# Kernel tuning notes

Measured on AMD Instinct MI355X. Metric: run time of the kernel, lower is better.

The kernel has to match this reference:

```python
import jax, jax.numpy as jnp
import numpy as np

SEQ_LEN = 4096
D_IN = 2048
D_OUT = 2048
DROPOUT_P = 0.5


def setup_inputs() -> dict:
    key = jax.random.key(0)
    kx, kq, kk, kv = jax.random.split(key, 4)
    return {
        "x": jax.random.normal(kx, (SEQ_LEN, D_IN), dtype=jnp.float32),
        "W_query": jax.random.uniform(kq, (D_IN, D_OUT), dtype=jnp.float32),
        "W_key": jax.random.uniform(kk, (D_IN, D_OUT), dtype=jnp.float32),
        "W_value": jax.random.uniform(kv, (D_IN, D_OUT), dtype=jnp.float32),
    }


def reference(x, W_query, W_key, W_value):
    # projections: [S, d_in] @ [d_in, d_out] -> [S, d_out]
    queries = x @ W_query
    keys = x @ W_key
    values = x @ W_value
    # full score matrix [S, S]
    attn_scores = queries @ keys.T
    S = attn_scores.shape[0]
    causal_mask = jnp.triu(jnp.ones((S, S), dtype=bool), k=1)
    masked = jnp.where(causal_mask, -jnp.inf, attn_scores)
    scale = jnp.sqrt(jnp.asarray(keys.shape[-1], dtype=masked.dtype))
    attn_weights = jax.nn.softmax(masked / scale, axis=1)
    # dropout p=0.5 (train mode), inverted scaling, deterministic key
    keep = jax.random.bernoulli(jax.random.key(42), 1.0 - DROPOUT_P, attn_weights.shape)
    attn_weights = jnp.where(keep, attn_weights / (1.0 - DROPOUT_P), 0.0)
    context_vec = attn_weights @ values  # [S, d_out]
    return context_vec
```

## Files before the change

### kernel.cpp

```cpp
#include <hip/hip_runtime.h>
#include <cstdint>
#include <cstddef>
#include <cmath>

#define SEQ 4096
#define DM  2048

typedef unsigned int u32;
typedef unsigned short u16;
typedef __attribute__((ext_vector_type(8))) short bf16x8;
typedef __attribute__((ext_vector_type(4))) float f32x4;

__device__ __forceinline__ u16 f2bf(float f) {
  u32 u = __float_as_uint(f);
  return (u16)((u + 0x7FFFu + ((u >> 16) & 1u)) >> 16);
}
__device__ __forceinline__ float bf2f(u16 h) { return __uint_as_float(((u32)h) << 16); }

__device__ __forceinline__ u32 rotl32(u32 x, int r) { return (x << r) | (x >> (32 - r)); }

__device__ __forceinline__ void tf2x32(u32 c0, u32 c1, u32& o0, u32& o1) {
  const u32 k0 = 0u, k1 = 42u, k2 = 0x1BD11BDAu ^ 0u ^ 42u;
  u32 x0 = c0 + k0;
  u32 x1 = c1 + k1;
#define TFR(r) { x0 += x1; x1 = rotl32(x1, (r)); x1 ^= x0; }
  TFR(13) TFR(15) TFR(26) TFR(6)   x0 += k1; x1 += k2 + 1u;
  TFR(17) TFR(29) TFR(16) TFR(24)  x0 += k2; x1 += k0 + 2u;
  TFR(13) TFR(15) TFR(26) TFR(6)   x0 += k0; x1 += k1 + 3u;
  TFR(17) TFR(29) TFR(16) TFR(24)  x0 += k1; x1 += k2 + 4u;
  TFR(13) TFR(15) TFR(26) TFR(6)   x0 += k2; x1 += k0 + 5u;
#undef TFR
  o0 = x0; o1 = x1;
}

__device__ __forceinline__ bool dropout_keep(u32 idx) {
  u32 a, b; tf2x32(0u, idx, a, b);
  return (((a ^ b) & 0x80000000u) == 0u);
}

__device__ __forceinline__ void g2l16(const void* g, void* l) {
  __builtin_amdgcn_global_load_lds((const __attribute__((address_space(1))) u32*)g,
                                   (__attribute__((address_space(3))) u32*)l, 16, 0, 0);
}

#define MFMA16(a, b, c) __builtin_amdgcn_mfma_f32_16x16x32_bf16(a, b, c, 0, 0, 0)


__device__ __forceinline__ void gemm_core_split(
    const u16* __restrict__ Ah, const u16* __restrict__ AlFT,
    const u16* __restrict__ Bh, const u16* __restrict__ BlFT,
    int lda, int ldb, int rowBlock, int colBlock, int kmax,
    f32x4 (&acc)[4][4], u16* smem)
{
  u16* Als = smem;
  u16* Bls = smem + 4096;
  const int tid  = threadIdx.x;
  const int wid  = tid >> 6;
  const int lane = tid & 63;
  const int wr   = (wid & 1) << 6;
  const int wc   = (wid >> 1) << 6;
  const int lrow = lane & 15;
  const int lk   = (((lane >> 4) ^ ((lrow >> 1) & 3)) << 3);
  const int srow = wid * 32 + (lane >> 2);
  const int skol = (((lane & 3) ^ ((lane >> 3) & 3)) << 3);
  const int KA32 = lda >> 5, KB32 = ldb >> 5;
  const int rtA = (rowBlock >> 4) + ((wid & 1) << 2);
  const int rtB = (colBlock >> 4) + ((wid >> 1) << 2);

  const f32x4 zero = {0.f, 0.f, 0.f, 0.f};
#pragma unroll
  for (int i = 0; i < 4; ++i)
#pragma unroll
    for (int j = 0; j < 4; ++j) acc[i][j] = zero;

  for (int kb = 0; kb < kmax; kb += 32) {
    const int kt = kb >> 5;
    bf16x8 al[4], bl[4];
#pragma unroll
    for (int r = 0; r < 4; ++r) {
      al[r] = *(const bf16x8*)(AlFT + (((size_t)(rtA + r) * KA32 + kt) * 64 + lane) * 8);
      bl[r] = *(const bf16x8*)(BlFT + (((size_t)(rtB + r) * KB32 + kt) * 64 + lane) * 8);
    }
#pragma unroll
    for (int t = 0; t < 2; ++t) {
      const size_t ga = (size_t)(rowBlock + srow + t * 16) * lda + kb + skol;
      const size_t gb = (size_t)(colBlock + srow + t * 16) * ldb + kb + skol;
      const int lo = (wid * 32 + t * 16) * 32;
      g2l16(Ah + ga, &Als[lo]);
      g2l16(Bh + gb, &Bls[lo]);
    }
    __syncthreads();

    bf16x8 ah[4], bh[4];
#pragma unroll
    for (int r = 0; r < 4; ++r) {
      ah[r] = *(const bf16x8*)&Als[(wr + r * 16 + lrow) * 32 + lk];
      bh[r] = *(const bf16x8*)&Bls[(wc + r * 16 + lrow) * 32 + lk];
    }
#pragma unroll
    for (int r = 0; r < 4; ++r)
#pragma unroll
      for (int c = 0; c < 4; ++c) {
        acc[r][c] = MFMA16(ah[r], bh[c], acc[r][c]);
        acc[r][c] = MFMA16(ah[r], bl[c], acc[r][c]);
        acc[r][c] = MFMA16(al[r], bh[c], acc[r][c]);
      }
    __syncthreads();
  }
}

__device__ __forceinline__ void gemm_core(
    const u16* __restrict__ Ah, const u16* __restrict__ Bh,
    int lda, int ldb, int rowBlock, int colBlock, int kmax,
    f32x4 (&acc)[4][4])
{
  __shared__ __align__(16) u16 Als[128 * 32];
  __shared__ __align__(16) u16 Bls[128 * 32];
  const int tid  = threadIdx.x;
  const int wid  = tid >> 6;
  const int lane = tid & 63;
  const int wr   = (wid & 1) << 6;
  const int wc   = (wid >> 1) << 6;
  const int lrow = lane & 15;
  const int lk   = (((lane >> 4) ^ ((lrow >> 1) & 3)) << 3);
  const int srow = wid * 32 + (lane >> 2);
  const int skol = (((lane & 3) ^ ((lane >> 3) & 3)) << 3);

  const f32x4 zero = {0.f, 0.f, 0.f, 0.f};
#pragma unroll
  for (int i = 0; i < 4; ++i)
#pragma unroll
    for (int j = 0; j < 4; ++j) acc[i][j] = zero;

  for (int kb = 0; kb < kmax; kb += 32) {
#pragma unroll
    for (int t = 0; t < 2; ++t) {
      const size_t ga = (size_t)(rowBlock + srow + t * 16) * lda + kb + skol;
      const size_t gb = (size_t)(colBlock + srow + t * 16) * ldb + kb + skol;
      const int lo = (wid * 32 + t * 16) * 32;
      g2l16(Ah + ga, &Als[lo]);
      g2l16(Bh + gb, &Bls[lo]);
    }
    __syncthreads();

    bf16x8 ah[4], bh[4];
#pragma unroll
    for (int r = 0; r < 4; ++r) {
      ah[r] = *(const bf16x8*)&Als[(wr + r * 16 + lrow) * 32 + lk];
      bh[r] = *(const bf16x8*)&Bls[(wc + r * 16 + lrow) * 32 + lk];
    }
#pragma unroll
    for (int r = 0; r < 4; ++r)
#pragma unroll
      for (int c = 0; c < 4; ++c)
        acc[r][c] = MFMA16(ah[r], bh[c], acc[r][c]);
    __syncthreads();
  }
}

__global__ __launch_bounds__(256) void k_split_x(const float* __restrict__ X,
                                                 u16* __restrict__ Xh, u16* __restrict__ Xl) {
  const int wid = threadIdx.x >> 6, lane = threadIdx.x & 63;
  const int kt = blockIdx.x;
  const int rt = blockIdx.y * 4 + wid;
  const int row = rt * 16 + (lane & 15);
  const int col = kt * 32 + ((lane >> 4) << 3);
  const float* src = X + (size_t)row * DM + col;
  const float4 v0 = *(const float4*)src;
  const float4 v1 = *(const float4*)(src + 4);
  float v[8] = {v0.x, v0.y, v0.z, v0.w, v1.x, v1.y, v1.z, v1.w};
  u16 h[8], l[8];
#pragma unroll
  for (int j = 0; j < 8; ++j) {
    h[j] = f2bf(v[j]);
    l[j] = f2bf(v[j] - bf2f(h[j]));
  }
  u16* hp = Xh + (size_t)row * DM + col;
  *(ushort4*)hp = *(ushort4*)&h[0];
  *(ushort4*)(hp + 4) = *(ushort4*)&h[4];
  u16* lp = Xl + (((size_t)rt * 64 + kt) * 64 + lane) * 8;
  *(ushort4*)lp = *(ushort4*)&l[0];
  *(ushort4*)(lp + 4) = *(ushort4*)&l[4];
}

__global__ __launch_bounds__(256) void k_split_w(
    const float* __restrict__ Wq, const float* __restrict__ Wk, const float* __restrict__ Wv,
    u16* __restrict__ Wqh, u16* __restrict__ Wql,
    u16* __restrict__ Wkh, u16* __restrict__ Wkl, u16* __restrict__ Wvh) {
  const int z = blockIdx.z;
  const float* W = (z == 0) ? Wq : (z == 1) ? Wk : Wv;
  u16* Oh = (z == 0) ? Wqh : (z == 1) ? Wkh : Wvh;
  u16* Ol = (z == 0) ? Wql : Wkl;
  __shared__ float t[64][65];
  const int tid = threadIdx.x;
  const int n0 = blockIdx.x * 64, k0 = blockIdx.y * 64;
  const int tx = tid & 63, ty = tid >> 6;
#pragma unroll
  for (int i = 0; i < 16; ++i)
    t[ty * 16 + i][tx] = W[(size_t)(k0 + ty * 16 + i) * DM + n0 + tx];
  __syncthreads();
  {
    const int nl = tid >> 2, kc = (tid & 3) * 16;
    u16 h[16];
#pragma unroll
    for (int i = 0; i < 16; ++i) h[i] = f2bf(t[kc + i][nl]);
    u16* hp = Oh + (size_t)(n0 + nl) * DM + k0 + kc;
#pragma unroll
    for (int i = 0; i < 4; ++i) *(ushort4*)(hp + i * 4) = *(ushort4*)&h[i * 4];
  }
  if (z < 2) {
    const int wid = tid >> 6, lane = tid & 63;
#pragma unroll
    for (int kt = 0; kt < 2; ++kt) {
      const int nl = wid * 16 + (lane & 15);
      const int kc = kt * 32 + ((lane >> 4) << 3);
      u16 l[8];
#pragma unroll
      for (int j = 0; j < 8; ++j) {
        const float v = t[kc + j][nl];
        l[j] = f2bf(v - bf2f(f2bf(v)));
      }
      const int rtg = (n0 >> 4) + wid, ktg = (k0 >> 5) + kt;
      u16* lp = Ol + (((size_t)rtg * 64 + ktg) * 64 + lane) * 8;
      *(ushort4*)lp = *(ushort4*)&l[0];
      *(ushort4*)(lp + 4) = *(ushort4*)&l[4];
    }
  }
}

__global__ __launch_bounds__(256) void k_proj_qk(
    const u16* __restrict__ Xh, const u16* __restrict__ Xl,
    const u16* __restrict__ Wqh, const u16* __restrict__ Wql,
    const u16* __restrict__ Wkh, const u16* __restrict__ Wkl,
    u16* __restrict__ Qh, u16* __restrict__ Ql,
    u16* __restrict__ Kh, u16* __restrict__ Kl, float rscaleQ)
{
  __shared__ __align__(16) u16 smem[128 * 128];
  const int z = blockIdx.z;
  const u16* Bh = z ? Wkh : Wqh;
  const u16* Bl = z ? Wkl : Wql;
  u16* Oh = z ? Kh : Qh;
  u16* Ol = z ? Kl : Ql;
  const float rs = z ? 1.0f : rscaleQ;
  const int rowBlock = blockIdx.y * 128, colBlock = blockIdx.x * 128;
  f32x4 acc[4][4];
  gemm_core_split(Xh, Xl, Bh, Bl, DM, DM, rowBlock, colBlock, DM, acc, smem);

  const int lane = threadIdx.x & 63, wid = threadIdx.x >> 6;
  const int lr0 = ((wid & 1) << 6) + ((lane >> 4) << 2);
  const int lc0 = ((wid >> 1) << 6) + (lane & 15);
#pragma unroll
  for (int r = 0; r < 4; ++r)
#pragma unroll
    for (int c = 0; c < 4; ++c)
#pragma unroll
      for (int e = 0; e < 4; ++e) {
        const float v = acc[r][c][e] * rs;
        const u16 h = f2bf(v);
        const int lrow = lr0 + r * 16 + e, lcol = lc0 + c * 16;
        Oh[(size_t)(rowBlock + lrow) * DM + colBlock + lcol] = h;
        smem[lrow * 128 + lcol] = f2bf(v - bf2f(h));
      }
  __syncthreads();
#pragma unroll
  for (int t8 = 0; t8 < 8; ++t8) {
    const int idx = wid * 8 + t8;
    const int rt = idx >> 2, kt = idx & 3;
    u16 l[8];
#pragma unroll
    for (int j = 0; j < 8; ++j)
      l[j] = smem[(rt * 16 + (lane & 15)) * 128 + kt * 32 + ((lane >> 4) << 3) + j];
    const int rtg = (rowBlock >> 4) + rt, ktg = (colBlock >> 5) + kt;
    u16* lp = Ol + (((size_t)rtg * (DM / 32) + ktg) * 64 + lane) * 8;
    *(ushort4*)lp = *(ushort4*)&l[0];
    *(ushort4*)(lp + 4) = *(ushort4*)&l[4];
  }
}

__global__ __launch_bounds__(256) void k_proj_v(
    const u16* __restrict__ Xh, const u16* __restrict__ Wvh, u16* __restrict__ Vt)
{
  f32x4 acc[4][4];
  gemm_core(Xh, Wvh, DM, DM, blockIdx.y * 128, blockIdx.x * 128, DM, acc);

  const int lane = threadIdx.x & 63, wid = threadIdx.x >> 6;
  const int r0 = blockIdx.y * 128 + ((wid & 1) << 6) + ((lane >> 4) << 2);
  const int c0 = blockIdx.x * 128 + ((wid >> 1) << 6) + (lane & 15);
#pragma unroll
  for (int r = 0; r < 4; ++r)
#pragma unroll
    for (int c = 0; c < 4; ++c) {
      const int d = c0 + c * 16;
      const int s0 = r0 + r * 16;
      ushort4 pk;
      pk.x = f2bf(acc[r][c][0]); pk.y = f2bf(acc[r][c][1]);
      pk.z = f2bf(acc[r][c][2]); pk.w = f2bf(acc[r][c][3]);
      *(ushort4*)(Vt + (size_t)d * SEQ + s0) = pk;
    }
}

__global__ __launch_bounds__(256) void k_scores(
    const u16* __restrict__ Qh, const u16* __restrict__ Ql,
    const u16* __restrict__ Kh, const u16* __restrict__ Kl, float* __restrict__ S)
{
  __shared__ __align__(16) u16 smem[128 * 64];
  const int bid = blockIdx.x;
  int by = (int)((sqrtf(8.0f * (float)bid + 1.0f) - 1.0f) * 0.5f);
  while ((by + 1) * (by + 2) / 2 <= bid) ++by;
  while (by * (by + 1) / 2 > bid) --by;
  const int bx = bid - by * (by + 1) / 2;

  f32x4 acc[4][4];
  gemm_core_split(Qh, Ql, Kh, Kl, DM, DM, by * 128, bx * 128, DM, acc, smem);

  const int lane = threadIdx.x & 63, wid = threadIdx.x >> 6;
  const int r0 = by * 128 + ((wid & 1) << 6) + ((lane >> 4) << 2);
  const int c0 = bx * 128 + ((wid >> 1) << 6) + (lane & 15);
#pragma unroll
  for (int r = 0; r < 4; ++r)
#pragma unroll
    for (int c = 0; c < 4; ++c)
#pragma unroll
      for (int e = 0; e < 4; ++e)
        S[(size_t)(r0 + r * 16 + e) * SEQ + (c0 + c * 16)] = acc[r][c][e];
}

__global__ __launch_bounds__(256) void k_softmax_dropout(const float* __restrict__ S,
                                                         u16* __restrict__ P) {
  const int row = blockIdx.x;
  const int n = row + 1;
  const int nt = (n + 1023) >> 10;
  const int tid = threadIdx.x;
  __shared__ float buf[SEQ];
  __shared__ float red[4];
  __shared__ float bcast;
  const float* srow = S + (size_t)row * SEQ;

  float lmax = -INFINITY;
  for (int t = 0; t < nt; ++t) {
    int j4 = tid + t * 256;
    float4 v = *(const float4*)(srow + (size_t)j4 * 4);
    int b = j4 * 4;
    float x0 = (b + 0 < n) ? v.x : -INFINITY;
    float x1 = (b + 1 < n) ? v.y : -INFINITY;
    float x2 = (b + 2 < n) ? v.z : -INFINITY;
    float x3 = (b + 3 < n) ? v.w : -INFINITY;
    buf[b + 0] = x0; buf[b + 1] = x1; buf[b + 2] = x2; buf[b + 3] = x3;
    lmax = fmaxf(lmax, fmaxf(fmaxf(x0, x1), fmaxf(x2, x3)));
  }
  for (int off = 32; off > 0; off >>= 1) lmax = fmaxf(lmax, __shfl_down(lmax, off, 64));
  if ((tid & 63) == 0) red[tid >> 6] = lmax;
  __syncthreads();
  if (tid == 0) bcast = fmaxf(fmaxf(red[0], red[1]), fmaxf(red[2], red[3]));
  __syncthreads();
  const float m = bcast;

  float lsum = 0.f;
  for (int t = 0; t < nt; ++t) {
    int b = (tid + t * 256) * 4;
    float e0 = expf(buf[b + 0] - m);
    float e1 = expf(buf[b + 1] - m);
    float e2 = expf(buf[b + 2] - m);
    float e3 = expf(buf[b + 3] - m);
    buf[b + 0] = e0; buf[b + 1] = e1; buf[b + 2] = e2; buf[b + 3] = e3;
    lsum += (e0 + e1) + (e2 + e3);
  }
  for (int off = 32; off > 0; off >>= 1) lsum += __shfl_down(lsum, off, 64);
  if ((tid & 63) == 0) red[tid >> 6] = lsum;
  __syncthreads();
  if (tid == 0) bcast = (red[0] + red[1]) + (red[2] + red[3]);
  __syncthreads();
  const float total = bcast;

  u16* prow = P + (size_t)row * SEQ;
  const int zeroEnd = ((row >> 7) + 1) << 7;
  for (int j = tid; j < zeroEnd; j += 256) {
    float out = 0.f;
    if (j < n) {
      const float w = buf[j] / total;
      out = dropout_keep((u32)(row * SEQ + j)) ? w * 2.0f : 0.f;
    }
    prow[j] = f2bf(out);
  }
}

__global__ __launch_bounds__(256) void k_pv(const u16* __restrict__ P,
                                            const u16* __restrict__ Vt,
                                            float* __restrict__ O) {
  const int by = (SEQ / 128 - 1) - blockIdx.y;
  f32x4 acc[4][4];
  gemm_core(P, Vt, SEQ, SEQ, by * 128, blockIdx.x * 128, (by + 1) * 128, acc);

  const int lane = threadIdx.x & 63, wid = threadIdx.x >> 6;
  const int r0 = by * 128 + ((wid & 1) << 6) + ((lane >> 4) << 2);
  const int c0 = blockIdx.x * 128 + ((wid >> 1) << 6) + (lane & 15);
#pragma unroll
  for (int r = 0; r < 4; ++r)
#pragma unroll
    for (int c = 0; c < 4; ++c)
#pragma unroll
      for (int e = 0; e < 4; ++e)
        O[(size_t)(r0 + r * 16 + e) * DM + (c0 + c * 16)] = acc[r][c][e];
}

extern "C" void kernel_launch(void* const* d_in, const int* in_sizes, int n_in,
                              void* d_out, int out_size, void* d_ws, size_t ws_size,
                              hipStream_t stream) {
  const float* x  = (const float*)d_in[0];
  const float* Wq = (const float*)d_in[1];
  const float* Wk = (const float*)d_in[2];
  const float* Wv = (const float*)d_in[3];

  const size_t PL = (size_t)SEQ * DM;
  const size_t WL = (size_t)DM * DM;
  u16* base = (u16*)d_ws;
  u16* Qh = base;
  u16* Ql = Qh + PL;
  u16* Kh = Ql + PL;
  u16* Kl = Kh + PL;
  u16* Vt = Kl + PL;
  u16* P  = base;
  u16* regA = Vt + PL;
  u16* Xh  = regA;
  u16* Xl  = Xh + PL;
  u16* Wqh = Xl + PL;
  u16* Wql = Wqh + WL;
  u16* Wkh = Wql + WL;
  u16* Wkl = Wkh + WL;
  u16* Wvh = Wkl + WL;
  float* S = (float*)regA;

  const float rscale = 1.0f / sqrtf(2048.0f);
  dim3 blk(256);
  k_split_x<<<dim3(DM / 32, SEQ / 64), blk, 0, stream>>>(x, Xh, Xl);
  k_split_w<<<dim3(DM / 64, DM / 64, 3), blk, 0, stream>>>(Wq, Wk, Wv, Wqh, Wql, Wkh, Wkl, Wvh);
  k_proj_qk<<<dim3(DM / 128, SEQ / 128, 2), blk, 0, stream>>>(Xh, Xl, Wqh, Wql, Wkh, Wkl,
                                                              Qh, Ql, Kh, Kl, rscale);
  k_proj_v<<<dim3(DM / 128, SEQ / 128), blk, 0, stream>>>(Xh, Wvh, Vt);
  k_scores<<<dim3((SEQ / 128) * (SEQ / 128 + 1) / 2), blk, 0, stream>>>(Qh, Ql, Kh, Kl, S);
  k_softmax_dropout<<<dim3(SEQ), blk, 0, stream>>>(S, P);
  k_pv<<<dim3(DM / 128, SEQ / 128), blk, 0, stream>>>(P, Vt, (float*)d_out);
}
```

Measured before the change: 681.5 us.

## Double K-step per barrier in GEMM cores and merge split/projection kernels

Both GEMM cores now stage two 32-wide K slices into LDS per iteration, a 64-wide K step, so they run half as many barrier pairs, at the cost of twice the shared memory. The split kernels for x and the weights are merged into one launch, and the V projection is folded into the Q/K projection kernel as a third z-slice. The aim is fewer launches and better occupancy and tail behaviour. The bigger LDS footprint may reduce how many blocks fit per CU.

```diff
diff --git a/kernel.cpp b/kernel.cpp
--- a/kernel.cpp
+++ b/kernel.cpp
@@ -5,6 +5,7 @@
 
 #define SEQ 4096
 #define DM  2048
+#define NSC ((SEQ / 128) * (SEQ / 128 + 1) / 2)
 
 typedef unsigned int u32;
 typedef unsigned short u16;
@@ -53,7 +54,7 @@
     f32x4 (&acc)[4][4], u16* smem)
 {
   u16* Als = smem;
-  u16* Bls = smem + 4096;
+  u16* Bls = smem + 8192;
   const int tid  = threadIdx.x;
   const int wid  = tid >> 6;
   const int lane = tid & 63;
@@ -73,38 +74,39 @@
 #pragma unroll
     for (int j = 0; j < 4; ++j) acc[i][j] = zero;
 
-  for (int kb = 0; kb < kmax; kb += 32) {
-    const int kt = kb >> 5;
-    bf16x8 al[4], bl[4];
-#pragma unroll
-    for (int r = 0; r < 4; ++r) {
-      al[r] = *(const bf16x8*)(AlFT + (((size_t)(rtA + r) * KA32 + kt) * 64 + lane) * 8);
-      bl[r] = *(const bf16x8*)(BlFT + (((size_t)(rtB + r) * KB32 + kt) * 64 + lane) * 8);
+  for (int kb = 0; kb < kmax; kb += 64) {
+#pragma unroll
+    for (int h = 0; h < 2; ++h)
+#pragma unroll
+      for (int t = 0; t < 2; ++t) {
+        const size_t ga = (size_t)(rowBlock + srow + t * 16) * lda + kb + h * 32 + skol;
+        const size_t gb = (size_t)(colBlock + srow + t * 16) * ldb + kb + h * 32 + skol;
+        const int lo = h * 4096 + (wid * 32 + t * 16) * 32;
+        g2l16(Ah + ga, &Als[lo]);
+        g2l16(Bh + gb, &Bls[lo]);
+      }
+    __syncthreads();
+
+#pragma unroll
+    for (int h = 0; h < 2; ++h) {
+      const int kt = (kb >> 5) + h;
+      bf16x8 al[4], bl[4], ah[4], bh[4];
+#pragma unroll
+      for (int r = 0; r < 4; ++r) {
+        al[r] = *(const bf16x8*)(AlFT + (((size_t)(rtA + r) * KA32 + kt) * 64 + lane) * 8);
+        bl[r] = *(const bf16x8*)(BlFT + (((size_t)(rtB + r) * KB32 + kt) * 64 + lane) * 8);
+        ah[r] = *(const bf16x8*)&Als[h * 4096 + (wr + r * 16 + lrow) * 32 + lk];
+        bh[r] = *(const bf16x8*)&Bls[h * 4096 + (wc + r * 16 + lrow) * 32 + lk];
+      }
+#pragma unroll
+      for (int r = 0; r < 4; ++r)
+#pragma unroll
+        for (int c = 0; c < 4; ++c) {
+          acc[r][c] = MFMA16(ah[r], bh[c], acc[r][c]);
+          acc[r][c] = MFMA16(ah[r], bl[c], acc[r][c]);
+          acc[r][c] = MFMA16(al[r], bh[c], acc[r][c]);
+        }
     }
-#pragma unroll
-    for (int t = 0; t < 2; ++t) {
-      const size_t ga = (size_t)(rowBlock + srow + t * 16) * lda + kb + skol;
-      const size_t gb = (size_t)(colBlock + srow + t * 16) * ldb + kb + skol;
-      const int lo = (wid * 32 + t * 16) * 32;
-      g2l16(Ah + ga, &Als[lo]);
-      g2l16(Bh + gb, &Bls[lo]);
-    }
-    __syncthreads();
-
-    bf16x8 ah[4], bh[4];
-#pragma unroll
-    for (int r = 0; r < 4; ++r) {
-      ah[r] = *(const bf16x8*)&Als[(wr + r * 16 + lrow) * 32 + lk];
-      bh[r] = *(const bf16x8*)&Bls[(wc + r * 16 + lrow) * 32 + lk];
-    }
-#pragma unroll
-    for (int r = 0; r < 4; ++r)
-#pragma unroll
-      for (int c = 0; c < 4; ++c) {
-        acc[r][c] = MFMA16(ah[r], bh[c], acc[r][c]);
-        acc[r][c] = MFMA16(ah[r], bl[c], acc[r][c]);
-        acc[r][c] = MFMA16(al[r], bh[c], acc[r][c]);
-      }
     __syncthreads();
   }
 }
@@ -112,10 +114,10 @@
 __device__ __forceinline__ void gemm_core(
     const u16* __restrict__ Ah, const u16* __restrict__ Bh,
     int lda, int ldb, int rowBlock, int colBlock, int kmax,
-    f32x4 (&acc)[4][4])
+    f32x4 (&acc)[4][4], u16* smem)
 {
-  __shared__ __align__(16) u16 Als[128 * 32];
-  __shared__ __align__(16) u16 Bls[128 * 32];
+  u16* Als = smem;
+  u16* Bls = smem + 8192;
   const int tid  = threadIdx.x;
   const int wid  = tid >> 6;
   const int lane = tid & 63;
@@ -132,68 +134,78 @@
 #pragma unroll
     for (int j = 0; j < 4; ++j) acc[i][j] = zero;
 
-  for (int kb = 0; kb < kmax; kb += 32) {
-#pragma unroll
-    for (int t = 0; t < 2; ++t) {
-      const size_t ga = (size_t)(rowBlock + srow + t * 16) * lda + kb + skol;
-      const size_t gb = (size_t)(colBlock + srow + t * 16) * ldb + kb + skol;
-      const int lo = (wid * 32 + t * 16) * 32;
-      g2l16(Ah + ga, &Als[lo]);
-      g2l16(Bh + gb, &Bls[lo]);
+  for (int kb = 0; kb < kmax; kb += 64) {
+#pragma unroll
+    for (int h = 0; h < 2; ++h)
+#pragma unroll
+      for (int t = 0; t < 2; ++t) {
+        const size_t ga = (size_t)(rowBlock + srow + t * 16) * lda + kb + h * 32 + skol;
+        const size_t gb = (size_t)(colBlock + srow + t * 16) * ldb + kb + h * 32 + skol;
+        const int lo = h * 4096 + (wid * 32 + t * 16) * 32;
+        g2l16(Ah + ga, &Als[lo]);
+        g2l16(Bh + gb, &Bls[lo]);
+      }
+    __syncthreads();
+
+#pragma unroll
+    for (int h = 0; h < 2; ++h) {
+      bf16x8 ah[4], bh[4];
+#pragma unroll
+      for (int r = 0; r < 4; ++r) {
+        ah[r] = *(const bf16x8*)&Als[h * 4096 + (wr + r * 16 + lrow) * 32 + lk];
+        bh[r] = *(const bf16x8*)&Bls[h * 4096 + (wc + r * 16 + lrow) * 32 + lk];
+      }
+#pragma unroll
+      for (int r = 0; r < 4; ++r)
+#pragma unroll
+        for (int c = 0; c < 4; ++c)
+          acc[r][c] = MFMA16(ah[r], bh[c], acc[r][c]);
     }
     __syncthreads();
-
-    bf16x8 ah[4], bh[4];
-#pragma unroll
-    for (int r = 0; r < 4; ++r) {
-      ah[r] = *(const bf16x8*)&Als[(wr + r * 16 + lrow) * 32 + lk];
-      bh[r] = *(const bf16x8*)&Bls[(wc + r * 16 + lrow) * 32 + lk];
-    }
-#pragma unroll
-    for (int r = 0; r < 4; ++r)
-#pragma unroll
-      for (int c = 0; c < 4; ++c)
-        acc[r][c] = MFMA16(ah[r], bh[c], acc[r][c]);
-    __syncthreads();
-  }
-}
-
-__global__ __launch_bounds__(256) void k_split_x(const float* __restrict__ X,
-                                                 u16* __restrict__ Xh, u16* __restrict__ Xl) {
-  const int wid = threadIdx.x >> 6, lane = threadIdx.x & 63;
-  const int kt = blockIdx.x;
-  const int rt = blockIdx.y * 4 + wid;
-  const int row = rt * 16 + (lane & 15);
-  const int col = kt * 32 + ((lane >> 4) << 3);
-  const float* src = X + (size_t)row * DM + col;
-  const float4 v0 = *(const float4*)src;
-  const float4 v1 = *(const float4*)(src + 4);
-  float v[8] = {v0.x, v0.y, v0.z, v0.w, v1.x, v1.y, v1.z, v1.w};
-  u16 h[8], l[8];
-#pragma unroll
-  for (int j = 0; j < 8; ++j) {
-    h[j] = f2bf(v[j]);
-    l[j] = f2bf(v[j] - bf2f(h[j]));
-  }
-  u16* hp = Xh + (size_t)row * DM + col;
-  *(ushort4*)hp = *(ushort4*)&h[0];
-  *(ushort4*)(hp + 4) = *(ushort4*)&h[4];
-  u16* lp = Xl + (((size_t)rt * 64 + kt) * 64 + lane) * 8;
-  *(ushort4*)lp = *(ushort4*)&l[0];
-  *(ushort4*)(lp + 4) = *(ushort4*)&l[4];
-}
-
-__global__ __launch_bounds__(256) void k_split_w(
+  }
+}
+
+__global__ __launch_bounds__(256) void k_split_all(
+    const float* __restrict__ X, u16* __restrict__ Xh, u16* __restrict__ Xl,
     const float* __restrict__ Wq, const float* __restrict__ Wk, const float* __restrict__ Wv,
     u16* __restrict__ Wqh, u16* __restrict__ Wql,
     u16* __restrict__ Wkh, u16* __restrict__ Wkl, u16* __restrict__ Wvh) {
-  const int z = blockIdx.z;
+  __shared__ float t[64][65];
+  const int bid = blockIdx.x;
+  const int tid = threadIdx.x;
+  const int wid = tid >> 6, lane = tid & 63;
+
+  if (bid < 4096) {
+    const int kt = bid & 63;
+    const int rt = (bid >> 6) * 4 + wid;
+    const int row = rt * 16 + (lane & 15);
+    const int col = kt * 32 + ((lane >> 4) << 3);
+    const float* src = X + (size_t)row * DM + col;
+    const float4 v0 = *(const float4*)src;
+    const float4 v1 = *(const float4*)(src + 4);
+    float v[8] = {v0.x, v0.y, v0.z, v0.w, v1.x, v1.y, v1.z, v1.w};
+    u16 h[8], l[8];
+#pragma unroll
+    for (int j = 0; j < 8; ++j) {
+      h[j] = f2bf(v[j]);
+      l[j] = f2bf(v[j] - bf2f(h[j]));
+    }
+    u16* hp = Xh + (size_t)row * DM + col;
+    *(ushort4*)hp = *(ushort4*)&h[0];
+    *(ushort4*)(hp + 4) = *(ushort4*)&h[4];
+    u16* lp = Xl + (((size_t)rt * 64 + kt) * 64 + lane) * 8;
+    *(ushort4*)lp = *(ushort4*)&l[0];
+    *(ushort4*)(lp + 4) = *(ushort4*)&l[4];
+    return;
+  }
+
+  const int r = bid - 4096;
+  const int z = r >> 10;
+  const int rem = r & 1023;
+  const int n0 = (rem & 31) * 64, k0 = (rem >> 5) * 64;
   const float* W = (z == 0) ? Wq : (z == 1) ? Wk : Wv;
   u16* Oh = (z == 0) ? Wqh : (z == 1) ? Wkh : Wvh;
   u16* Ol = (z == 0) ? Wql : Wkl;
-  __shared__ float t[64][65];
-  const int tid = threadIdx.x;
-  const int n0 = blockIdx.x * 64, k0 = blockIdx.y * 64;
   const int tx = tid & 63, ty = tid >> 6;
 #pragma unroll
   for (int i = 0; i < 16; ++i)
@@ -209,7 +221,6 @@
     for (int i = 0; i < 4; ++i) *(ushort4*)(hp + i * 4) = *(ushort4*)&h[i * 4];
   }
   if (z < 2) {
-    const int wid = tid >> 6, lane = tid & 63;
 #pragma unroll
     for (int kt = 0; kt < 2; ++kt) {
       const int nl = wid * 16 + (lane & 15);
@@ -228,25 +239,45 @@
   }
 }
 
-__global__ __launch_bounds__(256) void k_proj_qk(
+__global__ __launch_bounds__(256) void k_proj_qkv(
     const u16* __restrict__ Xh, const u16* __restrict__ Xl,
     const u16* __restrict__ Wqh, const u16* __restrict__ Wql,
     const u16* __restrict__ Wkh, const u16* __restrict__ Wkl,
+    const u16* __restrict__ Wvh,
     u16* __restrict__ Qh, u16* __restrict__ Ql,
-    u16* __restrict__ Kh, u16* __restrict__ Kl, float rscaleQ)
+    u16* __restrict__ Kh, u16* __restrict__ Kl,
+    u16* __restrict__ Vt, float rscaleQ)
 {
-  __shared__ __align__(16) u16 smem[128 * 128];
+  __shared__ __align__(16) u16 smem[16384];
   const int z = blockIdx.z;
+  const int rowBlock = blockIdx.y * 128, colBlock = blockIdx.x * 128;
+  const int lane = threadIdx.x & 63, wid = threadIdx.x >> 6;
+
+  if (z == 2) {
+    f32x4 acc[4][4];
+    gemm_core(Xh, Wvh, DM, DM, rowBlock, colBlock, DM, acc, smem);
+    const int r0 = rowBlock + ((wid & 1) << 6) + ((lane >> 4) << 2);
+    const int c0 = colBlock + ((wid >> 1) << 6) + (lane & 15);
+#pragma unroll
+    for (int r = 0; r < 4; ++r)
+#pragma unroll
+      for (int c = 0; c < 4; ++c) {
+        ushort4 pk;
+        pk.x = f2bf(acc[r][c][0]); pk.y = f2bf(acc[r][c][1]);
+        pk.z = f2bf(acc[r][c][2]); pk.w = f2bf(acc[r][c][3]);
+        *(ushort4*)(Vt + (size_t)(c0 + c * 16) * SEQ + r0 + r * 16) = pk;
+      }
+    return;
+  }
+
   const u16* Bh = z ? Wkh : Wqh;
   const u16* Bl = z ? Wkl : Wql;
   u16* Oh = z ? Kh : Qh;
   u16* Ol = z ? Kl : Ql;
   const float rs = z ? 1.0f : rscaleQ;
-  const int rowBlock = blockIdx.y * 128, colBlock = blockIdx.x * 128;
   f32x4 acc[4][4];
   gemm_core_split(Xh, Xl, Bh, Bl, DM, DM, rowBlock, colBlock, DM, acc, smem);
 
-  const int lane = threadIdx.x & 63, wid = threadIdx.x >> 6;
   const int lr0 = ((wid & 1) << 6) + ((lane >> 4) << 2);
   const int lc0 = ((wid >> 1) << 6) + (lane & 15);
 #pragma unroll
@@ -277,33 +308,11 @@
   }
 }
 
-__global__ __launch_bounds__(256) void k_proj_v(
-    const u16* __restrict__ Xh, const u16* __restrict__ Wvh, u16* __restrict__ Vt)
-{
-  f32x4 acc[4][4];
-  gemm_core(Xh, Wvh, DM, DM, blockIdx.y * 128, blockIdx.x * 128, DM, acc);
-
-  const int lane = threadIdx.x & 63, wid = threadIdx.x >> 6;
-  const int r0 = blockIdx.y * 128 + ((wid & 1) << 6) + ((lane >> 4) << 2);
-  const int c0 = blockIdx.x * 128 + ((wid >> 1) << 6) + (lane & 15);
-#pragma unroll
-  for (int r = 0; r < 4; ++r)
-#pragma unroll
-    for (int c = 0; c < 4; ++c) {
-      const int d = c0 + c * 16;
-      const int s0 = r0 + r * 16;
-      ushort4 pk;
-      pk.x = f2bf(acc[r][c][0]); pk.y = f2bf(acc[r][c][1]);
-      pk.z = f2bf(acc[r][c][2]); pk.w = f2bf(acc[r][c][3]);
-      *(ushort4*)(Vt + (size_t)d * SEQ + s0) = pk;
-    }
-}
-
 __global__ __launch_bounds__(256) void k_scores(
     const u16* __restrict__ Qh, const u16* __restrict__ Ql,
     const u16* __restrict__ Kh, const u16* __restrict__ Kl, float* __restrict__ S)
 {
-  __shared__ __align__(16) u16 smem[128 * 64];
+  __shared__ __align__(16) u16 smem[16384];
   const int bid = blockIdx.x;
   int by = (int)((sqrtf(8.0f * (float)bid + 1.0f) - 1.0f) * 0.5f);
   while ((by + 1) * (by + 2) / 2 <= bid) ++by;
@@ -387,9 +396,10 @@
 __global__ __launch_bounds__(256) void k_pv(const u16* __restrict__ P,
                                             const u16* __restrict__ Vt,
                                             float* __restrict__ O) {
+  __shared__ __align__(16) u16 smem[16384];
   const int by = (SEQ / 128 - 1) - blockIdx.y;
   f32x4 acc[4][4];
-  gemm_core(P, Vt, SEQ, SEQ, by * 128, blockIdx.x * 128, (by + 1) * 128, acc);
+  gemm_core(P, Vt, SEQ, SEQ, by * 128, blockIdx.x * 128, (by + 1) * 128, acc, smem);
 
   const int lane = threadIdx.x & 63, wid = threadIdx.x >> 6;
   const int r0 = by * 128 + ((wid & 1) << 6) + ((lane >> 4) << 2);
@@ -432,12 +442,11 @@
 
   const float rscale = 1.0f / sqrtf(2048.0f);
   dim3 blk(256);
-  k_split_x<<<dim3(DM / 32, SEQ / 64), blk, 0, stream>>>(x, Xh, Xl);
-  k_split_w<<<dim3(DM / 64, DM / 64, 3), blk, 0, stream>>>(Wq, Wk, Wv, Wqh, Wql, Wkh, Wkl, Wvh);
-  k_proj_qk<<<dim3(DM / 128, SEQ / 128, 2), blk, 0, stream>>>(Xh, Xl, Wqh, Wql, Wkh, Wkl,
-                                                              Qh, Ql, Kh, Kl, rscale);
-  k_proj_v<<<dim3(DM / 128, SEQ / 128), blk, 0, stream>>>(Xh, Wvh, Vt);
-  k_scores<<<dim3((SEQ / 128) * (SEQ / 128 + 1) / 2), blk, 0, stream>>>(Qh, Ql, Kh, Kl, S);
+  k_split_all<<<dim3(4096 + 3 * 1024), blk, 0, stream>>>(x, Xh, Xl, Wq, Wk, Wv,
+                                                         Wqh, Wql, Wkh, Wkl, Wvh);
+  k_proj_qkv<<<dim3(DM / 128, SEQ / 128, 3), blk, 0, stream>>>(
+      Xh, Xl, Wqh, Wql, Wkh, Wkl, Wvh, Qh, Ql, Kh, Kl, Vt, rscale);
+  k_scores<<<dim3(NSC), blk, 0, stream>>>(Qh, Ql, Kh, Kl, S);
   k_softmax_dropout<<<dim3(SEQ), blk, 0, stream>>>(S, P);
   k_pv<<<dim3(DM / 128, SEQ / 128), blk, 0, stream>>>(P, Vt, (float*)d_out);
 }
```

Measured after the change: 665.2 us. 2.4% less time.
